# Kernel tuning notes

Hardware: AMD Instinct MI355X
Metric: run time of the kernel (lower is better)

The kernel has to match this reference:

```python
import jax, jax.numpy as jnp
import numpy as np

S, H, A = 8192, 4096, 1024

def setup_inputs() -> dict:
    key = jax.random.key(0)
    ks = jax.random.split(key, 8)
    return {
        "encoder_outputs": jax.random.normal(ks[0], (S, H), jnp.float32),
        "hidden": jax.random.normal(ks[1], (H,), jnp.float32),
        "U_w": jax.random.normal(ks[2], (A, H), jnp.float32) * (1.0 / np.sqrt(H)),
        "U_b": jax.random.normal(ks[3], (A,), jnp.float32) * 0.01,
        "W_w": jax.random.normal(ks[4], (A, H), jnp.float32) * (1.0 / np.sqrt(H)),
        "W_b": jax.random.normal(ks[5], (A,), jnp.float32) * 0.01,
        "V_w": jax.random.normal(ks[6], (1, A), jnp.float32) * (1.0 / np.sqrt(A)),
        "V_b": jax.random.normal(ks[7], (1,), jnp.float32) * 0.01,
    }

def reference(encoder_outputs, hidden, U_w, U_b, W_w, W_b, V_w, V_b):
    # Bahdanau additive attention ('add' mode).
    W_hidden = hidden @ W_w.T + W_b                      # [A]
    U_encode = encoder_outputs @ U_w.T + U_b             # [S, A]
    poly_tanh = jnp.tanh(U_encode + W_hidden)            # [S, A]
    scores = poly_tanh @ V_w.T + V_b                     # [S, 1]
    attn = jax.nn.softmax(scores, axis=0)                # softmax over sequence
    context = attn.T @ encoder_outputs                   # [1, H]
    return context[None]                                 # [1, 1, H] (matches torch bmm)
```

## Files before the change

kernel.cpp:

```cpp
#include <hip/hip_runtime.h>

typedef __attribute__((ext_vector_type(8))) short short8;
typedef __attribute__((ext_vector_type(4))) float f32x4;

#define S_DIM 8192
#define H_DIM 4096
#define A_DIM 1024

__device__ __forceinline__ short f2bf(float x) {
  unsigned u = __float_as_uint(x);
  u += 0x7fffu + ((u >> 16) & 1u);
  return (short)(u >> 16);
}

__device__ __forceinline__ float bf2f(short b) {
  return __uint_as_float(((unsigned)(unsigned short)b) << 16);
}

__device__ __forceinline__ float fast_tanh(float x) {
  float e = __expf(-2.f * fabsf(x));
  float r = __fdividef(1.f - e, 1.f + e);
  return copysignf(r, x);
}

__device__ __forceinline__ void gload16(const void* g, void* l) {
  __builtin_amdgcn_global_load_lds(
      (const __attribute__((address_space(1))) void*)g,
      (__attribute__((address_space(3))) void*)l, 16, 0, 0);
}

__global__ __launch_bounds__(256) void comb_kernel(const float* __restrict__ hidden,
                                                   const float* __restrict__ Ww,
                                                   const float* __restrict__ Wb,
                                                   const float* __restrict__ Ub,
                                                   float* __restrict__ comb) {
  const int wave = threadIdx.x >> 6;
  const int lane = threadIdx.x & 63;
  const int a = blockIdx.x * 4 + wave;
  const float* row = Ww + (size_t)a * H_DIM;
  float acc = 0.f;
  for (int k = lane * 4; k < H_DIM; k += 64 * 4) {
    float4 w = *(const float4*)(row + k);
    float4 h = *(const float4*)(hidden + k);
    acc += w.x * h.x + w.y * h.y + w.z * h.z + w.w * h.w;
  }
  #pragma unroll
  for (int mk = 1; mk < 64; mk <<= 1) acc += __shfl_xor(acc, mk);
  if (lane == 0) comb[a] = acc + Wb[a] + Ub[a];
}

__global__ __launch_bounds__(256) void cvt_kernel(const float* __restrict__ src,
                                                  unsigned short* __restrict__ dst,
                                                  int n8) {
  const int stride = gridDim.x * blockDim.x;
  for (int i = blockIdx.x * blockDim.x + threadIdx.x; i < n8; i += stride) {
    float4 a = ((const float4*)src)[(size_t)i * 2];
    float4 b = ((const float4*)src)[(size_t)i * 2 + 1];
    short8 o;
    o[0] = f2bf(a.x); o[1] = f2bf(a.y); o[2] = f2bf(a.z); o[3] = f2bf(a.w);
    o[4] = f2bf(b.x); o[5] = f2bf(b.y); o[6] = f2bf(b.z); o[7] = f2bf(b.w);
    ((short8*)dst)[i] = o;
  }
}

__global__ __launch_bounds__(256) void gemm_kspl_kernel(
    const unsigned short* __restrict__ A,
    const unsigned short* __restrict__ B,
    unsigned short* __restrict__ partialC) {
  __shared__ __align__(16) unsigned short sA[128 * 64];
  __shared__ __align__(16) unsigned short sB[128 * 64];

  const int tid  = threadIdx.x;
  const int lane = tid & 63;
  const int wave = tid >> 6;
  const int wm = wave >> 1, wn = wave & 1;
  const int m0 = blockIdx.x * 128;
  const int n0 = blockIdx.y * 128;
  const int k0 = blockIdx.z * (H_DIM / 2);

  const int srow = wave * 32 + (lane >> 3);
  const int scol = (lane & 7) * 8;
  const unsigned short* ga = A + (size_t)(m0 + srow) * H_DIM + k0 + scol;
  const unsigned short* gb = B + (size_t)(n0 + srow) * H_DIM + k0 + scol;

  #define STAGE(kt) do {                                                     \
    const unsigned short* pa_ = ga + (size_t)(kt) * 64;                      \
    const unsigned short* pb_ = gb + (size_t)(kt) * 64;                      \
    _Pragma("unroll")                                                        \
    for (int i_ = 0; i_ < 4; ++i_) {                                         \
      gload16(pa_ + (size_t)i_ * 8 * H_DIM, &sA[(wave * 4 + i_) * 512]);     \
      gload16(pb_ + (size_t)i_ * 8 * H_DIM, &sB[(wave * 4 + i_) * 512]);     \
    }                                                                        \
  } while (0)

  f32x4 acc[4][4];
  const f32x4 zero = {0.f, 0.f, 0.f, 0.f};
  #pragma unroll
  for (int i = 0; i < 4; ++i)
    #pragma unroll
    for (int j = 0; j < 4; ++j) acc[i][j] = zero;

  STAGE(0);

  const int NK = (H_DIM / 2) / 64;
  for (int kt = 0; kt < NK; ++kt) {
    __syncthreads();

    short8 af[2][4], bfr[2][4];
    #pragma unroll
    for (int ks = 0; ks < 2; ++ks) {
      #pragma unroll
      for (int i = 0; i < 4; ++i)
        af[ks][i] = *(const short8*)&sA[(wm * 64 + i * 16 + (lane & 15)) * 64 + ks * 32 + (lane >> 4) * 8];
      #pragma unroll
      for (int j = 0; j < 4; ++j)
        bfr[ks][j] = *(const short8*)&sB[(wn * 64 + j * 16 + (lane & 15)) * 64 + ks * 32 + (lane >> 4) * 8];
    }
    __syncthreads();

    if (kt + 1 < NK) STAGE(kt + 1);

    #pragma unroll
    for (int ks = 0; ks < 2; ++ks)
      #pragma unroll
      for (int i = 0; i < 4; ++i)
        #pragma unroll
        for (int j = 0; j < 4; ++j)
          acc[i][j] = __builtin_amdgcn_mfma_f32_16x16x32_bf16(af[ks][i], bfr[ks][j], acc[i][j], 0, 0, 0);
  }
  #undef STAGE

  unsigned short* pc = partialC + (size_t)blockIdx.z * S_DIM * A_DIM;
  #pragma unroll
  for (int i = 0; i < 4; ++i) {
    #pragma unroll
    for (int r = 0; r < 4; ++r) {
      const int grow = m0 + wm * 64 + i * 16 + (lane >> 4) * 4 + r;
      unsigned short* prow = pc + (size_t)grow * A_DIM + n0 + wn * 64 + (lane & 15);
      #pragma unroll
      for (int j = 0; j < 4; ++j) prow[j * 16] = (unsigned short)f2bf(acc[i][j][r]);
    }
  }
}

__global__ __launch_bounds__(256) void tanh_score_kernel(
    const unsigned short* __restrict__ P,
    const float* __restrict__ comb,
    const float* __restrict__ Vw,
    float* __restrict__ scores) {
  const int lane = threadIdx.x & 63;
  const int wave = threadIdx.x >> 6;
  const int s = blockIdx.x * 4 + wave;
  const unsigned short* p0 = P + (size_t)s * A_DIM + lane * 16;
  const unsigned short* p1 = p0 + (size_t)S_DIM * A_DIM;

  short8 a0 = *(const short8*)(p0);
  short8 a1 = *(const short8*)(p0 + 8);
  short8 b0 = *(const short8*)(p1);
  short8 b1 = *(const short8*)(p1 + 8);
  float4 cb[4], vw[4];
  #pragma unroll
  for (int c = 0; c < 4; ++c) {
    cb[c] = *(const float4*)(comb + lane * 16 + c * 4);
    vw[c] = *(const float4*)(Vw + lane * 16 + c * 4);
  }

  float acc = 0.f;
  #pragma unroll
  for (int j = 0; j < 8; ++j) {
    float x = bf2f(a0[j]) + bf2f(b0[j]) + ((const float*)cb)[j];
    acc += ((const float*)vw)[j] * fast_tanh(x);
    float y = bf2f(a1[j]) + bf2f(b1[j]) + ((const float*)cb)[8 + j];
    acc += ((const float*)vw)[8 + j] * fast_tanh(y);
  }
  #pragma unroll
  for (int mk = 1; mk < 64; mk <<= 1) acc += __shfl_xor(acc, mk);
  if (lane == 0) scores[s] = acc;
}

__global__ __launch_bounds__(1024) void softmax_kernel(const float* __restrict__ scores,
                                                       float* __restrict__ attn) {
  __shared__ float redm[16];
  __shared__ float reds[16];
  const int tid = threadIdx.x;
  const int lane = tid & 63, wid = tid >> 6;
  float v[8];
  float m = -3.0e38f;
  #pragma unroll
  for (int i = 0; i < 8; ++i) { v[i] = scores[i * 1024 + tid]; m = fmaxf(m, v[i]); }
  #pragma unroll
  for (int mk = 1; mk < 64; mk <<= 1) m = fmaxf(m, __shfl_xor(m, mk));
  if (lane == 0) redm[wid] = m;
  __syncthreads();
  float M = redm[0];
  #pragma unroll
  for (int j = 1; j < 16; ++j) M = fmaxf(M, redm[j]);
  float e[8]; float s = 0.f;
  #pragma unroll
  for (int i = 0; i < 8; ++i) { e[i] = __expf(v[i] - M); s += e[i]; }
  #pragma unroll
  for (int mk = 1; mk < 64; mk <<= 1) s += __shfl_xor(s, mk);
  if (lane == 0) reds[wid] = s;
  __syncthreads();
  float T = 0.f;
  #pragma unroll
  for (int j = 0; j < 16; ++j) T += reds[j];
  const float inv = 1.f / T;
  #pragma unroll
  for (int i = 0; i < 8; ++i) attn[i * 1024 + tid] = e[i] * inv;
}

__global__ __launch_bounds__(256) void context_bf_kernel(const unsigned short* __restrict__ Ebf,
                                                         const float* __restrict__ attn,
                                                         float* __restrict__ partial) {
  const int h0 = (blockIdx.x * 256 + threadIdx.x) * 8;
  const int s0 = blockIdx.y * 64;
  float acc[8] = {0.f, 0.f, 0.f, 0.f, 0.f, 0.f, 0.f, 0.f};
  for (int s = s0; s < s0 + 64; ++s) {
    const float w = attn[s];
    short8 e = *(const short8*)(Ebf + (size_t)s * H_DIM + h0);
    #pragma unroll
    for (int j = 0; j < 8; ++j) acc[j] += w * bf2f(e[j]);
  }
  float* p = partial + (size_t)blockIdx.y * H_DIM + h0;
  #pragma unroll
  for (int j = 0; j < 8; ++j) p[j] = acc[j];
}

__global__ __launch_bounds__(256) void context_reduce_kernel(const float* __restrict__ partial,
                                                             float* __restrict__ out) {
  const int h = blockIdx.x * 256 + threadIdx.x;
  float acc = 0.f;
  #pragma unroll 8
  for (int y = 0; y < 128; ++y) acc += partial[(size_t)y * H_DIM + h];
  out[h] = acc;
}


__global__ __launch_bounds__(256) void gemm_score_bf_kernel(
    const unsigned short* __restrict__ A,
    const unsigned short* __restrict__ B,
    const float* __restrict__ comb,
    const float* __restrict__ Vw,
    float* __restrict__ scores) {
  __shared__ __align__(16) unsigned short sA[128 * 64];
  __shared__ __align__(16) unsigned short sB[128 * 64];
  const int tid  = threadIdx.x;
  const int lane = tid & 63;
  const int wave = tid >> 6;
  const int wm = wave >> 1, wn = wave & 1;
  const int m0 = blockIdx.x * 128;
  const int n0 = blockIdx.y * 128;
  const int srow = wave * 32 + (lane >> 3);
  const int scol = (lane & 7) * 8;
  const unsigned short* ga = A + (size_t)(m0 + srow) * H_DIM + scol;
  const unsigned short* gb = B + (size_t)(n0 + srow) * H_DIM + scol;
  #define STAGE(kt) do {                                                     \
    const unsigned short* pa_ = ga + (size_t)(kt) * 64;                      \
    const unsigned short* pb_ = gb + (size_t)(kt) * 64;                      \
    _Pragma("unroll")                                                        \
    for (int i_ = 0; i_ < 4; ++i_) {                                         \
      gload16(pa_ + (size_t)i_ * 8 * H_DIM, &sA[(wave * 4 + i_) * 512]);     \
      gload16(pb_ + (size_t)i_ * 8 * H_DIM, &sB[(wave * 4 + i_) * 512]);     \
    }                                                                        \
  } while (0)
  f32x4 acc[4][4];
  const f32x4 zero = {0.f, 0.f, 0.f, 0.f};
  #pragma unroll
  for (int i = 0; i < 4; ++i)
    #pragma unroll
    for (int j = 0; j < 4; ++j) acc[i][j] = zero;
  STAGE(0);
  const int NK = H_DIM / 64;
  for (int kt = 0; kt < NK; ++kt) {
    __syncthreads();
    short8 af[2][4], bfr[2][4];
    #pragma unroll
    for (int ks = 0; ks < 2; ++ks) {
      #pragma unroll
      for (int i = 0; i < 4; ++i)
        af[ks][i] = *(const short8*)&sA[(wm * 64 + i * 16 + (lane & 15)) * 64 + ks * 32 + (lane >> 4) * 8];
      #pragma unroll
      for (int j = 0; j < 4; ++j)
        bfr[ks][j] = *(const short8*)&sB[(wn * 64 + j * 16 + (lane & 15)) * 64 + ks * 32 + (lane >> 4) * 8];
    }
    __syncthreads();
    if (kt + 1 < NK) STAGE(kt + 1);
    #pragma unroll
    for (int ks = 0; ks < 2; ++ks)
      #pragma unroll
      for (int i = 0; i < 4; ++i)
        #pragma unroll
        for (int j = 0; j < 4; ++j)
          acc[i][j] = __builtin_amdgcn_mfma_f32_16x16x32_bf16(af[ks][i], bfr[ks][j], acc[i][j], 0, 0, 0);
  }
  #undef STAGE
  float vwv[4], cbv[4];
  #pragma unroll
  for (int j = 0; j < 4; ++j) {
    const int col = n0 + wn * 64 + j * 16 + (lane & 15);
    vwv[j] = Vw[col];
    cbv[j] = comb[col];
  }
  #pragma unroll
  for (int i = 0; i < 4; ++i) {
    #pragma unroll
    for (int r = 0; r < 4; ++r) {
      float s = 0.f;
      #pragma unroll
      for (int j = 0; j < 4; ++j)
        s += vwv[j] * fast_tanh(acc[i][j][r] + cbv[j]);
      s += __shfl_xor(s, 1);
      s += __shfl_xor(s, 2);
      s += __shfl_xor(s, 4);
      s += __shfl_xor(s, 8);
      if ((lane & 15) == 0) {
        const int grow = m0 + wm * 64 + i * 16 + (lane >> 4) * 4 + r;
        atomicAdd(&scores[grow], s);
      }
    }
  }
}


extern "C" void kernel_launch(void* const* d_in, const int* in_sizes, int n_in,
                              void* d_out, int out_size, void* d_ws, size_t ws_size,
                              hipStream_t stream) {
  const float* E   = (const float*)d_in[0];
  const float* hid = (const float*)d_in[1];
  const float* Uw  = (const float*)d_in[2];
  const float* Ub  = (const float*)d_in[3];
  const float* Ww  = (const float*)d_in[4];
  const float* Wb  = (const float*)d_in[5];
  const float* Vw  = (const float*)d_in[6];

  float* out    = (float*)d_out;
  float* ws     = (float*)d_ws;
  float* comb   = ws;
  float* scores = ws + 1024;
  float* attn   = ws + 1024 + 8192;
  float* ctxp   = ws + 17408;
  const size_t CTXP = (size_t)128 * H_DIM;

  unsigned short* pC    = (unsigned short*)(ws + 17408 + CTXP);
  unsigned short* Ebf2  = pC + 2 * (size_t)S_DIM * A_DIM;
  unsigned short* Uwbf2 = Ebf2 + (size_t)S_DIM * H_DIM;
  const size_t NEED2 = ((size_t)17408 + CTXP) * 4
                     + 2 * (size_t)S_DIM * A_DIM * 2
                     + ((size_t)S_DIM + A_DIM) * H_DIM * 2;

  unsigned short* Ebf1  = (unsigned short*)(ws + 17408 + CTXP);
  unsigned short* Uwbf1 = Ebf1 + (size_t)S_DIM * H_DIM;
  const size_t NEED1 = ((size_t)17408 + CTXP) * 4
                     + ((size_t)S_DIM + A_DIM) * H_DIM * 2;

  comb_kernel<<<A_DIM / 4, 256, 0, stream>>>(hid, Ww, Wb, Ub, comb);

  if (ws_size >= NEED2) {
    cvt_kernel<<<2048, 256, 0, stream>>>(E, Ebf2, (int)((size_t)S_DIM * H_DIM / 8));
    cvt_kernel<<<512, 256, 0, stream>>>(Uw, Uwbf2, (int)((size_t)A_DIM * H_DIM / 8));

    gemm_kspl_kernel<<<dim3(S_DIM / 128, A_DIM / 128, 2), 256, 0, stream>>>(Ebf2, Uwbf2, pC);
    tanh_score_kernel<<<S_DIM / 4, 256, 0, stream>>>(pC, comb, Vw, scores);

    softmax_kernel<<<1, 1024, 0, stream>>>(scores, attn);

    context_bf_kernel<<<dim3(H_DIM / 2048, S_DIM / 64), 256, 0, stream>>>(Ebf2, attn, ctxp);
    context_reduce_kernel<<<H_DIM / 256, 256, 0, stream>>>(ctxp, out);
  } else {
    hipMemsetAsync(scores, 0, S_DIM * sizeof(float), stream);
    cvt_kernel<<<2048, 256, 0, stream>>>(E, Ebf1, (int)((size_t)S_DIM * H_DIM / 8));
    cvt_kernel<<<512, 256, 0, stream>>>(Uw, Uwbf1, (int)((size_t)A_DIM * H_DIM / 8));

    gemm_score_bf_kernel<<<dim3(S_DIM / 128, A_DIM / 128), 256, 0, stream>>>(Ebf1, Uwbf1, comb, Vw, scores);
    softmax_kernel<<<1, 1024, 0, stream>>>(scores, attn);
    context_bf_kernel<<<dim3(H_DIM / 2048, S_DIM / 64), 256, 0, stream>>>(Ebf1, attn, ctxp);
    context_reduce_kernel<<<H_DIM / 256, 256, 0, stream>>>(ctxp, out);
  }
}
```

Baseline: 164.2 us.

## Fuse tanh-score epilogue into split-K GEMM via last-arriver atomic ticket

The split-K GEMM now keeps its accumulators and uses a per-tile atomic ticket. Whichever of the two K-halves finishes second reads the other half's bf16 partial, adds the bias, applies tanh, weights by V, and atomically adds per-row scores. This removes the separate tanh_score kernel and its re-read of both partial buffers. In exchange it adds memsets for the scores and tick arrays, thread fences, and float atomics into scores, which make the summation order nondeterministic.

```diff
diff --git a/kernel.cpp b/kernel.cpp
--- a/kernel.cpp
+++ b/kernel.cpp
@@ -63,10 +63,14 @@
   }
 }
 
-__global__ __launch_bounds__(256) void gemm_kspl_kernel(
+__global__ __launch_bounds__(256) void gemm_kspl_fin_kernel(
     const unsigned short* __restrict__ A,
     const unsigned short* __restrict__ B,
-    unsigned short* __restrict__ partialC) {
+    const float* __restrict__ comb,
+    const float* __restrict__ Vw,
+    unsigned short* __restrict__ pC,
+    int* __restrict__ tick,
+    float* __restrict__ scores) {
   __shared__ __align__(16) unsigned short sA[128 * 64];
   __shared__ __align__(16) unsigned short sB[128 * 64];
 
@@ -130,7 +134,7 @@
   }
   #undef STAGE
 
-  unsigned short* pc = partialC + (size_t)blockIdx.z * S_DIM * A_DIM;
+  unsigned short* pc = pC + (size_t)blockIdx.z * S_DIM * A_DIM;
   #pragma unroll
   for (int i = 0; i < 4; ++i) {
     #pragma unroll
@@ -141,41 +145,43 @@
       for (int j = 0; j < 4; ++j) prow[j * 16] = (unsigned short)f2bf(acc[i][j][r]);
     }
   }
-}
-
-__global__ __launch_bounds__(256) void tanh_score_kernel(
-    const unsigned short* __restrict__ P,
-    const float* __restrict__ comb,
-    const float* __restrict__ Vw,
-    float* __restrict__ scores) {
-  const int lane = threadIdx.x & 63;
-  const int wave = threadIdx.x >> 6;
-  const int s = blockIdx.x * 4 + wave;
-  const unsigned short* p0 = P + (size_t)s * A_DIM + lane * 16;
-  const unsigned short* p1 = p0 + (size_t)S_DIM * A_DIM;
-
-  short8 a0 = *(const short8*)(p0);
-  short8 a1 = *(const short8*)(p0 + 8);
-  short8 b0 = *(const short8*)(p1);
-  short8 b1 = *(const short8*)(p1 + 8);
-  float4 cb[4], vw[4];
-  #pragma unroll
-  for (int c = 0; c < 4; ++c) {
-    cb[c] = *(const float4*)(comb + lane * 16 + c * 4);
-    vw[c] = *(const float4*)(Vw + lane * 16 + c * 4);
-  }
-
-  float acc = 0.f;
-  #pragma unroll
-  for (int j = 0; j < 8; ++j) {
-    float x = bf2f(a0[j]) + bf2f(b0[j]) + ((const float*)cb)[j];
-    acc += ((const float*)vw)[j] * fast_tanh(x);
-    float y = bf2f(a1[j]) + bf2f(b1[j]) + ((const float*)cb)[8 + j];
-    acc += ((const float*)vw)[8 + j] * fast_tanh(y);
-  }
-  #pragma unroll
-  for (int mk = 1; mk < 64; mk <<= 1) acc += __shfl_xor(acc, mk);
-  if (lane == 0) scores[s] = acc;
+
+  __threadfence();
+  __syncthreads();
+  __shared__ int role;
+  if (tid == 0)
+    role = atomicAdd(&tick[blockIdx.x * (A_DIM / 128) + blockIdx.y], 1);
+  __syncthreads();
+  if (role == 0) return;
+  __threadfence();
+
+  const unsigned short* qc = pC + (size_t)(blockIdx.z ^ 1) * S_DIM * A_DIM;
+  float vwv[4], cbv[4];
+  #pragma unroll
+  for (int j = 0; j < 4; ++j) {
+    const int col = n0 + wn * 64 + j * 16 + (lane & 15);
+    vwv[j] = Vw[col];
+    cbv[j] = comb[col];
+  }
+  #pragma unroll
+  for (int i = 0; i < 4; ++i) {
+    #pragma unroll
+    for (int r = 0; r < 4; ++r) {
+      const int grow = m0 + wm * 64 + i * 16 + (lane >> 4) * 4 + r;
+      const unsigned short* qrow = qc + (size_t)grow * A_DIM + n0 + wn * 64 + (lane & 15);
+      float s = 0.f;
+      #pragma unroll
+      for (int j = 0; j < 4; ++j) {
+        float x = acc[i][j][r] + bf2f(qrow[j * 16]) + cbv[j];
+        s += vwv[j] * fast_tanh(x);
+      }
+      s += __shfl_xor(s, 1);
+      s += __shfl_xor(s, 2);
+      s += __shfl_xor(s, 4);
+      s += __shfl_xor(s, 8);
+      if ((lane & 15) == 0) atomicAdd(&scores[grow], s);
+    }
+  }
 }
 
 __global__ __launch_bounds__(1024) void softmax_kernel(const float* __restrict__ scores,
@@ -338,21 +344,25 @@
   float* ws     = (float*)d_ws;
   float* comb   = ws;
   float* scores = ws + 1024;
-  float* attn   = ws + 1024 + 8192;
-  float* ctxp   = ws + 17408;
+  float* attn   = ws + 9216;
+  int*   tick   = (int*)(ws + 17408);
+  float* ctxp   = ws + 17920;
   const size_t CTXP = (size_t)128 * H_DIM;
 
-  unsigned short* pC    = (unsigned short*)(ws + 17408 + CTXP);
+  unsigned short* pC    = (unsigned short*)(ws + 17920 + CTXP);
   unsigned short* Ebf2  = pC + 2 * (size_t)S_DIM * A_DIM;
   unsigned short* Uwbf2 = Ebf2 + (size_t)S_DIM * H_DIM;
-  const size_t NEED2 = ((size_t)17408 + CTXP) * 4
+  const size_t NEED2 = ((size_t)17920 + CTXP) * 4
                      + 2 * (size_t)S_DIM * A_DIM * 2
                      + ((size_t)S_DIM + A_DIM) * H_DIM * 2;
 
-  unsigned short* Ebf1  = (unsigned short*)(ws + 17408 + CTXP);
+  unsigned short* Ebf1  = (unsigned short*)(ws + 17920 + CTXP);
   unsigned short* Uwbf1 = Ebf1 + (size_t)S_DIM * H_DIM;
-  const size_t NEED1 = ((size_t)17408 + CTXP) * 4
+  const size_t NEED1 = ((size_t)17920 + CTXP) * 4
                      + ((size_t)S_DIM + A_DIM) * H_DIM * 2;
+
+  hipMemsetAsync(scores, 0, S_DIM * sizeof(float), stream);
+  hipMemsetAsync(tick, 0, 512 * sizeof(int), stream);
 
   comb_kernel<<<A_DIM / 4, 256, 0, stream>>>(hid, Ww, Wb, Ub, comb);
 
@@ -360,15 +370,14 @@
     cvt_kernel<<<2048, 256, 0, stream>>>(E, Ebf2, (int)((size_t)S_DIM * H_DIM / 8));
     cvt_kernel<<<512, 256, 0, stream>>>(Uw, Uwbf2, (int)((size_t)A_DIM * H_DIM / 8));
 
-    gemm_kspl_kernel<<<dim3(S_DIM / 128, A_DIM / 128, 2), 256, 0, stream>>>(Ebf2, Uwbf2, pC);
-    tanh_score_kernel<<<S_DIM / 4, 256, 0, stream>>>(pC, comb, Vw, scores);
+    gemm_kspl_fin_kernel<<<dim3(S_DIM / 128, A_DIM / 128, 2), 256, 0, stream>>>(
+        Ebf2, Uwbf2, comb, Vw, pC, tick, scores);
 
     softmax_kernel<<<1, 1024, 0, stream>>>(scores, attn);
 
     context_bf_kernel<<<dim3(H_DIM / 2048, S_DIM / 64), 256, 0, stream>>>(Ebf2, attn, ctxp);
     context_reduce_kernel<<<H_DIM / 256, 256, 0, stream>>>(ctxp, out);
   } else {
-    hipMemsetAsync(scores, 0, S_DIM * sizeof(float), stream);
     cvt_kernel<<<2048, 256, 0, stream>>>(E, Ebf1, (int)((size_t)S_DIM * H_DIM / 8));
     cvt_kernel<<<512, 256, 0, stream>>>(Uw, Uwbf1, (int)((size_t)A_DIM * H_DIM / 8));
 
```

Result: slower. 380.4 us (+131.6%).
